# Kernel optimization log

Hardware: AMD Instinct MI355X
Metric: run time of the kernel (lower is better)

Reference implementation:

```python
import jax, jax.numpy as jnp
import numpy as np

N = 100000   # nodes
E = 400000   # edges
G = 2000     # graphs in batch
F0 = 84      # num_features_xd
F2 = 840     # num_features_xd * 10


def setup_inputs() -> dict:
    key = jax.random.key(0)
    ks = jax.random.split(key, 8)
    x = jax.random.normal(ks[0], (N, F0), dtype=jnp.float32)
    edge_index = jax.random.randint(ks[1], (2, E), 0, N)
    batch = jnp.sort(jax.random.randint(ks[2], (N,), 0, G))

    def lin(k, fan_in, fan_out):
        bound = 1.0 / np.sqrt(fan_in)
        kw, kb = jax.random.split(k)
        W = jax.random.uniform(kw, (fan_in, fan_out), jnp.float32, -bound, bound)
        b = jax.random.uniform(kb, (fan_out,), jnp.float32, -bound, bound)
        return W, b

    W1, b1 = lin(ks[3], F0, F0)          # GINConv.nn of conv1
    W2, b2 = lin(ks[4], F0, F2)          # GINConv.nn of conv2
    Wf1, bf1 = lin(ks[5], 2 * F2, 1024)  # fc_g[0]
    Wf2, bf2 = lin(ks[6], 1024, 384)     # fc_g[3]
    return dict(x=x, edge_index=edge_index, batch=batch,
                W1=W1, b1=b1, W2=W2, b2=b2,
                Wf1=Wf1, bf1=bf1, Wf2=Wf2, bf2=bf2)


def _gin_conv(h, src, dst, W, b):
    # GINConv with default eps=0: nn((1+eps)*h + sum_{j in N(i)} h_j)
    agg = jax.ops.segment_sum(h[src], dst, num_segments=N)  # scatter-add over edges
    return (h + agg) @ W + b


def reference(x, edge_index, batch, W1, b1, W2, b2, Wf1, bf1, Wf2, bf2):
    src, dst = edge_index[0], edge_index[1]
    h1 = jax.nn.relu(_gin_conv(x, src, dst, W1, b1))    # [N, 84]
    h2 = jax.nn.relu(_gin_conv(h1, src, dst, W2, b2))   # [N, 840]
    # global_max_pool / global_add_pool over graphs
    pool_max = jax.ops.segment_max(h2, batch, num_segments=G)  # [G, 840]
    pool_sum = jax.ops.segment_sum(h2, batch, num_segments=G)  # [G, 840]
    xg = jnp.concatenate([pool_max, pool_sum], axis=1)          # [G, 1680]
    # fc_g: Linear->ReLU->(Dropout=id in eval)->Linear
    xg = jax.nn.relu(xg @ Wf1 + bf1) @ Wf2 + bf2                # [G, 384]
    return (xg, h2)
```

## Files before the change

kernel.cpp:

```cpp
#include <hip/hip_runtime.h>
#include <math.h>

#define NN 100000
#define NE 400000
#define NG 2000
#define F0 84
#define F2 840
#define FH 1024
#define FO 384

typedef __attribute__((ext_vector_type(8))) short bf16x8;
typedef __attribute__((ext_vector_type(4))) float f32x4;

__device__ inline short f2bf(float f) {
    union { float f; unsigned u; } v; v.f = f;
    unsigned r = (v.u + 0x7FFFu + ((v.u >> 16) & 1u)) >> 16;
    return (short)r;
}
__device__ inline float b2f(short s) {
    union { unsigned u; float f; } v;
    v.u = ((unsigned)(unsigned short)s) << 16;
    return v.f;
}

#define S1 (6*3*64)
#define S2 (56*3*64)
#define S3 (64*53*64)
#define S4 (24*32*64)
#define PACK_TOT (S1 + S2 + S3 + S4)
#define NB_DEG  1563
#define NB_CAST 4688
#define NB_PACK 1087

__device__ inline void pack_one(const float* __restrict__ W, short* __restrict__ P,
                                int K, int N, int KB, int CT, int idx) {
    int lane = idx & 63;
    int t    = idx >> 6;
    int kb   = t % KB;
    int ct   = t / KB;
    int col  = ct * 16 + (lane & 15);
    int k0   = kb * 32 + ((lane >> 4) << 3);
    bf16x8 v;
#pragma unroll
    for (int j = 0; j < 8; ++j) {
        int k = k0 + j;
        float f = (k < K && col < N) ? W[(size_t)k * N + col] : 0.f;
        v[j] = f2bf(f);
    }
    *reinterpret_cast<bf16x8*>(P + (size_t)idx * 8) = v;
}

__global__ void front_kernel(const int* __restrict__ dst, int* __restrict__ deg,
                             const float* __restrict__ x, short* __restrict__ Xb,
                             const float* __restrict__ W1, short* __restrict__ P1,
                             const float* __restrict__ W2, short* __restrict__ P2,
                             const float* __restrict__ Wf1, short* __restrict__ P3,
                             const float* __restrict__ Wf2, short* __restrict__ P4) {
    int bid = blockIdx.x;
    if (bid < NB_DEG) {
        int e = bid * 256 + threadIdx.x;
        if (e < NE) atomicAdd(&deg[dst[e]], 1);
        return;
    }
    bid -= NB_DEG;
    if (bid < NB_CAST) {
        int idx = bid * 256 + threadIdx.x;
        if (idx < NN * 12) {
            int n = idx / 12;
            int c = idx - n * 12;
            int k0 = c * 8;
            bf16x8 v;
#pragma unroll
            for (int j = 0; j < 8; ++j) {
                int k = k0 + j;
                v[j] = (k < F0) ? f2bf(x[(size_t)n * F0 + k]) : (short)0;
            }
            *reinterpret_cast<bf16x8*>(Xb + (size_t)n * 96 + k0) = v;
        }
        return;
    }
    bid -= NB_CAST;
    int idx = bid * 256 + threadIdx.x;
    if (idx < S1) { pack_one(W1, P1, F0, F0, 3, 6, idx); return; }
    idx -= S1;
    if (idx < S2) { pack_one(W2, P2, F0, F2, 3, 56, idx); return; }
    idx -= S2;
    if (idx < S3) { pack_one(Wf1, P3, 1680, FH, 53, 64, idx); return; }
    idx -= S3;
    if (idx < S4) { pack_one(Wf2, P4, FH, FO, 32, 24, idx); return; }
}

__global__ void scan_ph1(const int* __restrict__ deg, int* __restrict__ rowptr,
                         int* __restrict__ bsum) {
    __shared__ int s[1024];
    int t = threadIdx.x;
    int i = blockIdx.x * 1024 + t;
    int v = (i < NN) ? deg[i] : 0;
    s[t] = v;
    __syncthreads();
    for (int d = 1; d < 1024; d <<= 1) {
        int u = (t >= d) ? s[t - d] : 0;
        __syncthreads();
        s[t] += u;
        __syncthreads();
    }
    if (i < NN) rowptr[i] = s[t] - v;
    if (t == 1023) bsum[blockIdx.x] = s[t];
}

__global__ void scan_ph23(int* __restrict__ rowptr, const int* __restrict__ bsum,
                          int nb) {
    __shared__ int s[128];
    int t = threadIdx.x;
    int b = blockIdx.x;
    if (t < 128) s[t] = (t < b && t < nb) ? bsum[t] : 0;
    __syncthreads();
    for (int d = 64; d >= 1; d >>= 1) {
        if (t < d) s[t] += s[t + d];
        __syncthreads();
    }
    int off = s[0];
    int i = b * 1024 + t;
    if (i < NN) rowptr[i] += off;
    if (i == 0) rowptr[NN] = NE;
}

__global__ void edge_fill(const int* __restrict__ src, const int* __restrict__ dst,
                          const int* __restrict__ rowptr, int* __restrict__ cnt,
                          int* __restrict__ eid) {
    int e = blockIdx.x * blockDim.x + threadIdx.x;
    if (e >= NE) return;
    int d = dst[e];
    int p = rowptr[d] + atomicAdd(&cnt[d], 1);
    eid[p] = src[e];
}

template <int CTW, int NWAVES, bool OUTBF16>
__global__ void conv_fused(const short* __restrict__ H,
                           const int* __restrict__ rowptr,
                           const int* __restrict__ eid,
                           const short* __restrict__ Bp,
                           const float* __restrict__ bias,
                           void* __restrict__ Cout,
                           int Nbias, int ldc, int ncols) {
    __shared__ short Alds[3 * 512];
    int rt = blockIdx.x;
    int t  = threadIdx.x;

    for (int item = t; item < 192; item += NWAVES * 64) {
        int r = item / 12;
        int c = item - r * 12;
        int n = rt * 16 + r;
        int off = c * 8;
        bf16x8 sv = *reinterpret_cast<const bf16x8*>(H + (size_t)n * 96 + off);
        float acc[8];
#pragma unroll
        for (int j = 0; j < 8; ++j) acc[j] = b2f(sv[j]);
        int e0 = rowptr[n], e1 = rowptr[n + 1];
        for (int e = e0; e < e1; ++e) {
            int s = eid[e];
            bf16x8 v = *reinterpret_cast<const bf16x8*>(H + (size_t)s * 96 + off);
#pragma unroll
            for (int j = 0; j < 8; ++j) acc[j] += b2f(v[j]);
        }
        bf16x8 o;
#pragma unroll
        for (int j = 0; j < 8; ++j) o[j] = f2bf(acc[j]);
        int kb = c >> 2, q = c & 3;
        *reinterpret_cast<bf16x8*>(&Alds[(kb * 512) + (q * 16 + r) * 8]) = o;
    }
    __syncthreads();

    int wave = t >> 6;
    int lane = t & 63;
    f32x4 acc[CTW];
#pragma unroll
    for (int u = 0; u < CTW; ++u) acc[u] = (f32x4){0.f, 0.f, 0.f, 0.f};
    const short* Bbase = Bp + (size_t)(wave * CTW) * 3 * 512 + lane * 8;
#pragma unroll
    for (int kb = 0; kb < 3; ++kb) {
        bf16x8 a = *reinterpret_cast<const bf16x8*>(&Alds[kb * 512 + lane * 8]);
#pragma unroll
        for (int u = 0; u < CTW; ++u) {
            bf16x8 b = *reinterpret_cast<const bf16x8*>(Bbase + ((size_t)u * 3 + kb) * 512);
            acc[u] = __builtin_amdgcn_mfma_f32_16x16x32_bf16(a, b, acc[u], 0, 0, 0);
        }
    }
    int row0 = rt * 16 + ((lane >> 4) << 2);
#pragma unroll
    for (int u = 0; u < CTW; ++u) {
        int col = (wave * CTW + u) * 16 + (lane & 15);
        float bi = (col < Nbias) ? bias[col] : 0.f;
        if (col < ncols) {
#pragma unroll
            for (int r = 0; r < 4; ++r) {
                float v = fmaxf(acc[u][r] + bi, 0.f);
                if (OUTBF16) ((short*)Cout)[(size_t)(row0 + r) * ldc + col] = f2bf(v);
                else         ((float*)Cout)[(size_t)(row0 + r) * ldc + col] = v;
            }
        }
    }
}

template <int CTW, bool RELU, bool OUTBF16>
__global__ void gemmN(const short* __restrict__ A, const short* __restrict__ Bp,
                      const float* __restrict__ bias, void* __restrict__ Cout,
                      int Kp, int Nbias, int ldc, int ncols,
                      int rowTiles, int ctGroups) {
    int gid = blockIdx.x * blockDim.x + threadIdx.x;
    int w   = gid >> 6;
    if (w >= rowTiles * ctGroups) return;
    int lane = gid & 63;
    int rt = w / ctGroups;
    int cg = w - rt * ctGroups;
    int KB = Kp >> 5;
    const short* Ap = A + (size_t)(rt * 16 + (lane & 15)) * Kp + ((lane >> 4) << 3);
    const short* Bbase = Bp + (size_t)(cg * CTW) * KB * 512 + lane * 8;
    f32x4 acc[CTW];
#pragma unroll
    for (int u = 0; u < CTW; ++u) acc[u] = (f32x4){0.f, 0.f, 0.f, 0.f};
    for (int kb = 0; kb < KB; ++kb) {
        bf16x8 a = *reinterpret_cast<const bf16x8*>(Ap + kb * 32);
#pragma unroll
        for (int u = 0; u < CTW; ++u) {
            bf16x8 b = *reinterpret_cast<const bf16x8*>(Bbase + ((size_t)u * KB + kb) * 512);
            acc[u] = __builtin_amdgcn_mfma_f32_16x16x32_bf16(a, b, acc[u], 0, 0, 0);
        }
    }
    int row0 = rt * 16 + ((lane >> 4) << 2);
#pragma unroll
    for (int u = 0; u < CTW; ++u) {
        int col = (cg * CTW + u) * 16 + (lane & 15);
        float bi = (col < Nbias) ? bias[col] : 0.f;
        if (col < ncols) {
#pragma unroll
            for (int r = 0; r < 4; ++r) {
                int row = row0 + r;
                float v = acc[u][r] + bi;
                if (RELU) v = fmaxf(v, 0.f);
                if (OUTBF16) ((short*)Cout)[(size_t)row * ldc + col] = f2bf(v);
                else         ((float*)Cout)[(size_t)row * ldc + col] = v;
            }
        }
    }
}

__global__ void pool_kernel(const float* __restrict__ h2,
                            const int* __restrict__ batch,
                            short* __restrict__ A3) {
    int g = blockIdx.x;
    int t = threadIdx.x;
    __shared__ int se[2];
    if (t < 2) {
        int target = g + t;
        int lo = 0, hi = NN;
        while (lo < hi) {
            int mid = (lo + hi) >> 1;
            if (batch[mid] < target) lo = mid + 1; else hi = mid;
        }
        se[t] = lo;
    }
    __syncthreads();
    int s = se[0], e = se[1];
    if (t < 210) {
        int c4 = t * 4;
        float sm0 = 0.f, sm1 = 0.f, sm2 = 0.f, sm3 = 0.f;
        float mx0 = -INFINITY, mx1 = -INFINITY, mx2 = -INFINITY, mx3 = -INFINITY;
        for (int n = s; n < e; ++n) {
            float4 v = *reinterpret_cast<const float4*>(h2 + (size_t)n * F2 + c4);
            sm0 += v.x; sm1 += v.y; sm2 += v.z; sm3 += v.w;
            mx0 = fmaxf(mx0, v.x); mx1 = fmaxf(mx1, v.y);
            mx2 = fmaxf(mx2, v.z); mx3 = fmaxf(mx3, v.w);
        }
        short* xr = A3 + (size_t)g * 1696;
        short4 mo, so;
        mo.x = f2bf(mx0); mo.y = f2bf(mx1); mo.z = f2bf(mx2); mo.w = f2bf(mx3);
        so.x = f2bf(sm0); so.y = f2bf(sm1); so.z = f2bf(sm2); so.w = f2bf(sm3);
        *reinterpret_cast<short4*>(xr + c4)      = mo;
        *reinterpret_cast<short4*>(xr + F2 + c4) = so;
    }
    if (t >= 210 && t < 214) {
        short4 z = {0, 0, 0, 0};
        *reinterpret_cast<short4*>(A3 + (size_t)g * 1696 + 1680 + (t - 210) * 4) = z;
    }
}

extern "C" void kernel_launch(void* const* d_in, const int* in_sizes, int n_in,
                              void* d_out, int out_size, void* d_ws, size_t ws_size,
                              hipStream_t stream) {
    const float* x    = (const float*)d_in[0];
    const int*   ei   = (const int*)d_in[1];
    const int*   batch= (const int*)d_in[2];
    const float* W1   = (const float*)d_in[3];
    const float* b1   = (const float*)d_in[4];
    const float* W2   = (const float*)d_in[5];
    const float* b2   = (const float*)d_in[6];
    const float* Wf1  = (const float*)d_in[7];
    const float* bf1  = (const float*)d_in[8];
    const float* Wf2  = (const float*)d_in[9];
    const float* bf2  = (const float*)d_in[10];

    const int* src = ei;
    const int* dst = ei + NE;

    float* xg_out = (float*)d_out;
    float* h2     = (float*)d_out + (size_t)NG * FO;

    short* Xb   = (short*)d_ws;
    short* h1   = Xb + (size_t)NN * 96;
    short* A3   = h1 + (size_t)NN * 96;
    short* fc1o = A3 + (size_t)NG * 1696;
    short* W1p  = fc1o + (size_t)NG * FH;
    short* W2p  = W1p + (size_t)S1 * 8;
    short* Wf1p = W2p + (size_t)S2 * 8;
    short* Wf2p = Wf1p + (size_t)S3 * 8;
    int*   deg  = (int*)(Wf2p + (size_t)S4 * 8);
    int*   cnt  = deg + NN;
    int*   rowptr = cnt + NN;
    int*   bsum = rowptr + NN + 1;
    int*   eid  = bsum + 128;

    const int blk = 256;
    auto cdiv = [](long long a, long long b) { return (int)((a + b - 1) / b); };
    const int nb1024 = cdiv(NN, 1024);

    hipMemsetAsync(deg, 0, 2 * (size_t)NN * sizeof(int), stream);
    front_kernel<<<NB_DEG + NB_CAST + NB_PACK, blk, 0, stream>>>(
        dst, deg, x, Xb, W1, W1p, W2, W2p, Wf1, Wf1p, Wf2, Wf2p);

    scan_ph1<<<nb1024, 1024, 0, stream>>>(deg, rowptr, bsum);
    scan_ph23<<<nb1024, 1024, 0, stream>>>(rowptr, bsum, nb1024);
    edge_fill<<<cdiv(NE, blk), blk, 0, stream>>>(src, dst, rowptr, cnt, eid);

    conv_fused<6, 1, true><<<6250, 64, 0, stream>>>(
        Xb, rowptr, eid, W1p, b1, h1, F0, 96, 96);

    conv_fused<14, 4, false><<<6250, 256, 0, stream>>>(
        h1, rowptr, eid, W2p, b2, h2, F2, F2, F2);

    pool_kernel<<<NG, blk, 0, stream>>>(h2, batch, A3);

    gemmN<2, true, true><<<cdiv(125LL * 32 * 64, blk), blk, 0, stream>>>(
        A3, Wf1p, bf1, fc1o, 1696, FH, FH, FH, 125, 32);
    gemmN<2, false, false><<<cdiv(125LL * 12 * 64, blk), blk, 0, stream>>>(
        fc1o, Wf2p, bf2, xg_out, 1024, FO, FO, FO, 125, 12);
}
```

Measured before the change: 396.1 us.

## Fuse second GIN conv with per-graph max/sum pooling in one kernel

```diff
diff --git a/kernel.cpp b/kernel.cpp
--- a/kernel.cpp
+++ b/kernel.cpp
@@ -200,6 +200,117 @@
             }
         }
     }
+}
+
+__global__ __launch_bounds__(256) void conv2_pool(
+        const short* __restrict__ H, const int* __restrict__ rowptr,
+        const int* __restrict__ eid, const int* __restrict__ batch,
+        const short* __restrict__ Bp, const float* __restrict__ bias,
+        float* __restrict__ h2, short* __restrict__ A3) {
+    __shared__ short Alds[3 * 512];
+    __shared__ int se[2];
+    int g = blockIdx.x;
+    int t = threadIdx.x;
+    if (t < 2) {
+        int target = g + t;
+        int lo = 0, hi = NN;
+        while (lo < hi) {
+            int mid = (lo + hi) >> 1;
+            if (batch[mid] < target) lo = mid + 1; else hi = mid;
+        }
+        se[t] = lo;
+    }
+    __syncthreads();
+    int s = se[0], e = se[1];
+    int wave = t >> 6, lane = t & 63;
+    const short* Bbase = Bp + (size_t)(wave * 14) * 3 * 512 + lane * 8;
+
+    float pmax[14], psum[14];
+#pragma unroll
+    for (int u = 0; u < 14; ++u) { pmax[u] = -INFINITY; psum[u] = 0.f; }
+
+    int nch = (e - s + 15) >> 4;
+    for (int ch = 0; ch < nch; ++ch) {
+        int base = s + ch * 16;
+        if (t < 192) {
+            int r = t / 12, c = t - r * 12;
+            int n = base + r;
+            int kb = c >> 2, q = c & 3;
+            short* slot = &Alds[kb * 512 + (q * 16 + r) * 8];
+            if (n < e) {
+                int off = c * 8;
+                bf16x8 sv = *reinterpret_cast<const bf16x8*>(H + (size_t)n * 96 + off);
+                float acc[8];
+#pragma unroll
+                for (int j = 0; j < 8; ++j) acc[j] = b2f(sv[j]);
+                int e0 = rowptr[n], e1 = rowptr[n + 1];
+                for (int ed = e0; ed < e1; ++ed) {
+                    int sr = eid[ed];
+                    bf16x8 v = *reinterpret_cast<const bf16x8*>(H + (size_t)sr * 96 + off);
+#pragma unroll
+                    for (int j = 0; j < 8; ++j) acc[j] += b2f(v[j]);
+                }
+                bf16x8 o;
+#pragma unroll
+                for (int j = 0; j < 8; ++j) o[j] = f2bf(acc[j]);
+                *reinterpret_cast<bf16x8*>(slot) = o;
+            } else {
+                bf16x8 z = {0, 0, 0, 0, 0, 0, 0, 0};
+                *reinterpret_cast<bf16x8*>(slot) = z;
+            }
+        }
+        __syncthreads();
+
+        f32x4 acc[14];
+#pragma unroll
+        for (int u = 0; u < 14; ++u) acc[u] = (f32x4){0.f, 0.f, 0.f, 0.f};
+#pragma unroll
+        for (int kb = 0; kb < 3; ++kb) {
+            bf16x8 a = *reinterpret_cast<const bf16x8*>(&Alds[kb * 512 + lane * 8]);
+#pragma unroll
+            for (int u = 0; u < 14; ++u) {
+                bf16x8 b = *reinterpret_cast<const bf16x8*>(Bbase + ((size_t)u * 3 + kb) * 512);
+                acc[u] = __builtin_amdgcn_mfma_f32_16x16x32_bf16(a, b, acc[u], 0, 0, 0);
+            }
+        }
+        int rg = base + ((lane >> 4) << 2);
+#pragma unroll
+        for (int u = 0; u < 14; ++u) {
+            int col = (wave * 14 + u) * 16 + (lane & 15);
+            if (col < F2) {
+                float bi = bias[col];
+                float m = -INFINITY, sm = 0.f;
+#pragma unroll
+                for (int r = 0; r < 4; ++r) {
+                    int row = rg + r;
+                    if (row < e) {
+                        float v = fmaxf(acc[u][r] + bi, 0.f);
+                        h2[(size_t)row * F2 + col] = v;
+                        m = fmaxf(m, v);
+                        sm += v;
+                    }
+                }
+                pmax[u] = fmaxf(pmax[u], m);
+                psum[u] += sm;
+            }
+        }
+        __syncthreads();
+    }
+
+#pragma unroll
+    for (int u = 0; u < 14; ++u) {
+        float m = pmax[u], sm = psum[u];
+        m = fmaxf(m, __shfl_xor(m, 16));
+        m = fmaxf(m, __shfl_xor(m, 32));
+        sm += __shfl_xor(sm, 16);
+        sm += __shfl_xor(sm, 32);
+        int col = (wave * 14 + u) * 16 + (lane & 15);
+        if (lane < 16 && col < F2) {
+            A3[(size_t)g * 1696 + col]      = f2bf(m);
+            A3[(size_t)g * 1696 + F2 + col] = f2bf(sm);
+        }
+    }
+    if (t < 16) A3[(size_t)g * 1696 + 1680 + t] = 0;
 }
 
 template <int CTW, bool RELU, bool OUTBF16>
@@ -245,46 +356,6 @@
     }
 }
 
-__global__ void pool_kernel(const float* __restrict__ h2,
-                            const int* __restrict__ batch,
-                            short* __restrict__ A3) {
-    int g = blockIdx.x;
-    int t = threadIdx.x;
-    __shared__ int se[2];
-    if (t < 2) {
-        int target = g + t;
-        int lo = 0, hi = NN;
-        while (lo < hi) {
-            int mid = (lo + hi) >> 1;
-            if (batch[mid] < target) lo = mid + 1; else hi = mid;
-        }
-        se[t] = lo;
-    }
-    __syncthreads();
-    int s = se[0], e = se[1];
-    if (t < 210) {
-        int c4 = t * 4;
-        float sm0 = 0.f, sm1 = 0.f, sm2 = 0.f, sm3 = 0.f;
-        float mx0 = -INFINITY, mx1 = -INFINITY, mx2 = -INFINITY, mx3 = -INFINITY;
-        for (int n = s; n < e; ++n) {
-            float4 v = *reinterpret_cast<const float4*>(h2 + (size_t)n * F2 + c4);
-            sm0 += v.x; sm1 += v.y; sm2 += v.z; sm3 += v.w;
-            mx0 = fmaxf(mx0, v.x); mx1 = fmaxf(mx1, v.y);
-            mx2 = fmaxf(mx2, v.z); mx3 = fmaxf(mx3, v.w);
-        }
-        short* xr = A3 + (size_t)g * 1696;
-        short4 mo, so;
-        mo.x = f2bf(mx0); mo.y = f2bf(mx1); mo.z = f2bf(mx2); mo.w = f2bf(mx3);
-        so.x = f2bf(sm0); so.y = f2bf(sm1); so.z = f2bf(sm2); so.w = f2bf(sm3);
-        *reinterpret_cast<short4*>(xr + c4)      = mo;
-        *reinterpret_cast<short4*>(xr + F2 + c4) = so;
-    }
-    if (t >= 210 && t < 214) {
-        short4 z = {0, 0, 0, 0};
-        *reinterpret_cast<short4*>(A3 + (size_t)g * 1696 + 1680 + (t - 210) * 4) = z;
-    }
-}
-
 extern "C" void kernel_launch(void* const* d_in, const int* in_sizes, int n_in,
                               void* d_out, int out_size, void* d_ws, size_t ws_size,
                               hipStream_t stream) {
@@ -335,10 +406,7 @@
     conv_fused<6, 1, true><<<6250, 64, 0, stream>>>(
         Xb, rowptr, eid, W1p, b1, h1, F0, 96, 96);
 
-    conv_fused<14, 4, false><<<6250, 256, 0, stream>>>(
-        h1, rowptr, eid, W2p, b2, h2, F2, F2, F2);
-
-    pool_kernel<<<NG, blk, 0, stream>>>(h2, batch, A3);
+    conv2_pool<<<NG, blk, 0, stream>>>(h1, rowptr, eid, batch, W2p, b2, h2, A3);
 
     gemmN<2, true, true><<<cdiv(125LL * 32 * 64, blk), blk, 0, stream>>>(
         A3, Wf1p, bf1, fc1o, 1696, FH, FH, FH, 125, 32);
```

After: 637.4 us. 1.61x slower.

## Fuse per-tile partial max/sum pooling into conv2 epilogue and widen conv1 launch

Applied to the files above, without the earlier changes.

```diff
diff --git a/kernel.cpp b/kernel.cpp
--- a/kernel.cpp
+++ b/kernel.cpp
@@ -8,6 +8,7 @@
 #define F2 840
 #define FH 1024
 #define FO 384
+#define NT2 6250
 
 typedef __attribute__((ext_vector_type(8))) short bf16x8;
 typedef __attribute__((ext_vector_type(4))) float f32x4;
@@ -23,14 +24,14 @@
     return v.f;
 }
 
-#define S1 (6*3*64)
+#define S1 (8*3*64)
 #define S2 (56*3*64)
 #define S3 (64*53*64)
 #define S4 (24*32*64)
 #define PACK_TOT (S1 + S2 + S3 + S4)
 #define NB_DEG  1563
 #define NB_CAST 4688
-#define NB_PACK 1087
+#define NB_PACK 1088
 
 __device__ inline void pack_one(const float* __restrict__ W, short* __restrict__ P,
                                 int K, int N, int KB, int CT, int idx) {
@@ -81,7 +82,7 @@
     }
     bid -= NB_CAST;
     int idx = bid * 256 + threadIdx.x;
-    if (idx < S1) { pack_one(W1, P1, F0, F0, 3, 6, idx); return; }
+    if (idx < S1) { pack_one(W1, P1, F0, F0, 3, 8, idx); return; }
     idx -= S1;
     if (idx < S2) { pack_one(W2, P2, F0, F2, 3, 56, idx); return; }
     idx -= S2;
@@ -199,6 +200,146 @@
                 else         ((float*)Cout)[(size_t)(row0 + r) * ldc + col] = v;
             }
         }
+    }
+}
+
+__global__ __launch_bounds__(256) void conv2_part(
+        const short* __restrict__ H, const int* __restrict__ rowptr,
+        const int* __restrict__ eid, const short* __restrict__ Bp,
+        const float* __restrict__ bias, float* __restrict__ h2,
+        float* __restrict__ Pmax, float* __restrict__ Psum) {
+    __shared__ short Alds[3 * 512];
+    int rt = blockIdx.x;
+    int t  = threadIdx.x;
+
+    for (int item = t; item < 192; item += 256) {
+        int r = item / 12;
+        int c = item - r * 12;
+        int n = rt * 16 + r;
+        int off = c * 8;
+        bf16x8 sv = *reinterpret_cast<const bf16x8*>(H + (size_t)n * 96 + off);
+        float acc[8];
+#pragma unroll
+        for (int j = 0; j < 8; ++j) acc[j] = b2f(sv[j]);
+        int e0 = rowptr[n], e1 = rowptr[n + 1];
+        for (int e = e0; e < e1; ++e) {
+            int s = eid[e];
+            bf16x8 v = *reinterpret_cast<const bf16x8*>(H + (size_t)s * 96 + off);
+#pragma unroll
+            for (int j = 0; j < 8; ++j) acc[j] += b2f(v[j]);
+        }
+        bf16x8 o;
+#pragma unroll
+        for (int j = 0; j < 8; ++j) o[j] = f2bf(acc[j]);
+        int kb = c >> 2, q = c & 3;
+        *reinterpret_cast<bf16x8*>(&Alds[(kb * 512) + (q * 16 + r) * 8]) = o;
+    }
+    __syncthreads();
+
+    int wave = t >> 6;
+    int lane = t & 63;
+    f32x4 acc[14];
+#pragma unroll
+    for (int u = 0; u < 14; ++u) acc[u] = (f32x4){0.f, 0.f, 0.f, 0.f};
+    const short* Bbase = Bp + (size_t)(wave * 14) * 3 * 512 + lane * 8;
+#pragma unroll
+    for (int kb = 0; kb < 3; ++kb) {
+        bf16x8 a = *reinterpret_cast<const bf16x8*>(&Alds[kb * 512 + lane * 8]);
+#pragma unroll
+        for (int u = 0; u < 14; ++u) {
+            bf16x8 b = *reinterpret_cast<const bf16x8*>(Bbase + ((size_t)u * 3 + kb) * 512);
+            acc[u] = __builtin_amdgcn_mfma_f32_16x16x32_bf16(a, b, acc[u], 0, 0, 0);
+        }
+    }
+    int row0 = rt * 16 + ((lane >> 4) << 2);
+#pragma unroll
+    for (int u = 0; u < 14; ++u) {
+        int col = (wave * 14 + u) * 16 + (lane & 15);
+        if (col < F2) {
+            float bi = bias[col];
+            float m = -INFINITY, sm = 0.f;
+#pragma unroll
+            for (int r = 0; r < 4; ++r) {
+                float v = fmaxf(acc[u][r] + bi, 0.f);
+                h2[(size_t)(row0 + r) * F2 + col] = v;
+                m = fmaxf(m, v);
+                sm += v;
+            }
+            m = fmaxf(m, __shfl_xor(m, 16));
+            m = fmaxf(m, __shfl_xor(m, 32));
+            sm += __shfl_xor(sm, 16);
+            sm += __shfl_xor(sm, 32);
+            if (lane < 16) {
+                Pmax[(size_t)rt * F2 + col] = m;
+                Psum[(size_t)rt * F2 + col] = sm;
+            }
+        }
+    }
+}
+
+__global__ void pool_kernel(const float* __restrict__ h2,
+                            const int* __restrict__ batch,
+                            const float* __restrict__ Pmax,
+                            const float* __restrict__ Psum,
+                            short* __restrict__ A3) {
+    int g = blockIdx.x;
+    int t = threadIdx.x;
+    __shared__ int se[2];
+    if (t < 2) {
+        int target = g + t;
+        int lo = 0, hi = NN;
+        while (lo < hi) {
+            int mid = (lo + hi) >> 1;
+            if (batch[mid] < target) lo = mid + 1; else hi = mid;
+        }
+        se[t] = lo;
+    }
+    __syncthreads();
+    int s = se[0], e = se[1];
+    int t0 = (s + 15) >> 4;
+    int t1 = e >> 4;
+    if (t < 210) {
+        int c4 = t * 4;
+        float sm0 = 0.f, sm1 = 0.f, sm2 = 0.f, sm3 = 0.f;
+        float mx0 = -INFINITY, mx1 = -INFINITY, mx2 = -INFINITY, mx3 = -INFINITY;
+        if (t1 >= t0) {
+            for (int tile = t0; tile < t1; ++tile) {
+                float4 pm = *reinterpret_cast<const float4*>(Pmax + (size_t)tile * F2 + c4);
+                float4 ps = *reinterpret_cast<const float4*>(Psum + (size_t)tile * F2 + c4);
+                mx0 = fmaxf(mx0, pm.x); mx1 = fmaxf(mx1, pm.y);
+                mx2 = fmaxf(mx2, pm.z); mx3 = fmaxf(mx3, pm.w);
+                sm0 += ps.x; sm1 += ps.y; sm2 += ps.z; sm3 += ps.w;
+            }
+            for (int n = s; n < (t0 << 4); ++n) {
+                float4 v = *reinterpret_cast<const float4*>(h2 + (size_t)n * F2 + c4);
+                sm0 += v.x; sm1 += v.y; sm2 += v.z; sm3 += v.w;
+                mx0 = fmaxf(mx0, v.x); mx1 = fmaxf(mx1, v.y);
+                mx2 = fmaxf(mx2, v.z); mx3 = fmaxf(mx3, v.w);
+            }
+            for (int n = (t1 << 4); n < e; ++n) {
+                float4 v = *reinterpret_cast<const float4*>(h2 + (size_t)n * F2 + c4);
+                sm0 += v.x; sm1 += v.y; sm2 += v.z; sm3 += v.w;
+                mx0 = fmaxf(mx0, v.x); mx1 = fmaxf(mx1, v.y);
+                mx2 = fmaxf(mx2, v.z); mx3 = fmaxf(mx3, v.w);
+            }
+        } else {
+            for (int n = s; n < e; ++n) {
+                float4 v = *reinterpret_cast<const float4*>(h2 + (size_t)n * F2 + c4);
+                sm0 += v.x; sm1 += v.y; sm2 += v.z; sm3 += v.w;
+                mx0 = fmaxf(mx0, v.x); mx1 = fmaxf(mx1, v.y);
+                mx2 = fmaxf(mx2, v.z); mx3 = fmaxf(mx3, v.w);
+            }
+        }
+        short* xr = A3 + (size_t)g * 1696;
+        short4 mo, so;
+        mo.x = f2bf(mx0); mo.y = f2bf(mx1); mo.z = f2bf(mx2); mo.w = f2bf(mx3);
+        so.x = f2bf(sm0); so.y = f2bf(sm1); so.z = f2bf(sm2); so.w = f2bf(sm3);
+        *reinterpret_cast<short4*>(xr + c4)      = mo;
+        *reinterpret_cast<short4*>(xr + F2 + c4) = so;
+    }
+    if (t >= 210 && t < 214) {
+        short4 z = {0, 0, 0, 0};
+        *reinterpret_cast<short4*>(A3 + (size_t)g * 1696 + 1680 + (t - 210) * 4) = z;
     }
 }
 
@@ -245,46 +386,6 @@
     }
 }
 
-__global__ void pool_kernel(const float* __restrict__ h2,
-                            const int* __restrict__ batch,
-                            short* __restrict__ A3) {
-    int g = blockIdx.x;
-    int t = threadIdx.x;
-    __shared__ int se[2];
-    if (t < 2) {
-        int target = g + t;
-        int lo = 0, hi = NN;
-        while (lo < hi) {
-            int mid = (lo + hi) >> 1;
-            if (batch[mid] < target) lo = mid + 1; else hi = mid;
-        }
-        se[t] = lo;
-    }
-    __syncthreads();
-    int s = se[0], e = se[1];
-    if (t < 210) {
-        int c4 = t * 4;
-        float sm0 = 0.f, sm1 = 0.f, sm2 = 0.f, sm3 = 0.f;
-        float mx0 = -INFINITY, mx1 = -INFINITY, mx2 = -INFINITY, mx3 = -INFINITY;
-        for (int n = s; n < e; ++n) {
-            float4 v = *reinterpret_cast<const float4*>(h2 + (size_t)n * F2 + c4);
-            sm0 += v.x; sm1 += v.y; sm2 += v.z; sm3 += v.w;
-            mx0 = fmaxf(mx0, v.x); mx1 = fmaxf(mx1, v.y);
-            mx2 = fmaxf(mx2, v.z); mx3 = fmaxf(mx3, v.w);
-        }
-        short* xr = A3 + (size_t)g * 1696;
-        short4 mo, so;
-        mo.x = f2bf(mx0); mo.y = f2bf(mx1); mo.z = f2bf(mx2); mo.w = f2bf(mx3);
-        so.x = f2bf(sm0); so.y = f2bf(sm1); so.z = f2bf(sm2); so.w = f2bf(sm3);
-        *reinterpret_cast<short4*>(xr + c4)      = mo;
-        *reinterpret_cast<short4*>(xr + F2 + c4) = so;
-    }
-    if (t >= 210 && t < 214) {
-        short4 z = {0, 0, 0, 0};
-        *reinterpret_cast<short4*>(A3 + (size_t)g * 1696 + 1680 + (t - 210) * 4) = z;
-    }
-}
-
 extern "C" void kernel_launch(void* const* d_in, const int* in_sizes, int n_in,
                               void* d_out, int out_size, void* d_ws, size_t ws_size,
                               hipStream_t stream) {
@@ -319,6 +420,8 @@
     int*   rowptr = cnt + NN;
     int*   bsum = rowptr + NN + 1;
     int*   eid  = bsum + 128;
+    float* Pmax = (float*)(eid + NE);
+    float* Psum = Pmax + (size_t)NT2 * F2;
 
     const int blk = 256;
     auto cdiv = [](long long a, long long b) { return (int)((a + b - 1) / b); };
@@ -332,13 +435,12 @@
     scan_ph23<<<nb1024, 1024, 0, stream>>>(rowptr, bsum, nb1024);
     edge_fill<<<cdiv(NE, blk), blk, 0, stream>>>(src, dst, rowptr, cnt, eid);
 
-    conv_fused<6, 1, true><<<6250, 64, 0, stream>>>(
+    conv_fused<2, 4, true><<<NT2, 256, 0, stream>>>(
         Xb, rowptr, eid, W1p, b1, h1, F0, 96, 96);
 
-    conv_fused<14, 4, false><<<6250, 256, 0, stream>>>(
-        h1, rowptr, eid, W2p, b2, h2, F2, F2, F2);
-
-    pool_kernel<<<NG, blk, 0, stream>>>(h2, batch, A3);
+    conv2_part<<<NT2, 256, 0, stream>>>(h1, rowptr, eid, W2p, b2, h2, Pmax, Psum);
+
+    pool_kernel<<<NG, blk, 0, stream>>>(h2, batch, Pmax, Psum, A3);
 
     gemmN<2, true, true><<<cdiv(125LL * 32 * 64, blk), blk, 0, stream>>>(
         A3, Wf1p, bf1, fc1o, 1696, FH, FH, FH, 125, 32);
```

New measurement: 364.7 us. 7.9% less time.
